# Kernel optimization log

Hardware: AMD Instinct MI355X
Metric: run time of the kernel (lower is better)

## Reference

```python
import jax, jax.numpy as jnp
import numpy as np
import math

B, L, DIM = 2, 2048, 1024
NUM_HEADS, QUANTUM_HEADS, CHUNK = 16, 2, 64
HD = DIM // NUM_HEADS  # 64 == CHUNK (required by the original broadcast)
TH = NUM_HEADS - QUANTUM_HEADS
STEPS = 2048
LN_EPS = 1e-5


def setup_inputs() -> dict:
    key = jax.random.key(0)
    ks = jax.random.split(key, 12)
    inp = {
        'x': jax.random.normal(ks[0], (B, L, DIM), dtype=jnp.float32),
        # to_quantum_state: Linear(HD, 2HD) + LayerNorm(2HD) + Tanh
        'wq1': jax.random.normal(ks[1], (HD, 2 * HD), dtype=jnp.float32) * 0.05,
        'bq1': jnp.zeros((2 * HD,), dtype=jnp.float32),
        'ln_g': jnp.ones((2 * HD,), dtype=jnp.float32),
        'ln_b': jnp.zeros((2 * HD,), dtype=jnp.float32),
        'phase_shifts': jax.random.normal(ks[2], (QUANTUM_HEADS,), dtype=jnp.float32) * 0.02,
        'freqs': jax.random.normal(ks[3], (QUANTUM_HEADS,), dtype=jnp.float32) * 0.02,
        # traditional heads: q/k/v projections, no bias
        'wq': jax.random.normal(ks[4], (DIM, TH * HD), dtype=jnp.float32) * 0.02,
        'wk': jax.random.normal(ks[5], (DIM, TH * HD), dtype=jnp.float32) * 0.02,
        'wv': jax.random.normal(ks[6], (DIM, TH * HD), dtype=jnp.float32) * 0.02,
        # output projection
        'wo': jax.random.normal(ks[7], (DIM, DIM), dtype=jnp.float32) * 0.02,
        'bo': jnp.zeros((DIM,), dtype=jnp.float32),
    }
    return inp


def _quantum_state(t, wq1, bq1, ln_g, ln_b):
    # Linear -> LayerNorm -> Tanh; split into (amp, phase)
    h = t @ wq1 + bq1
    mu = h.mean(-1, keepdims=True)
    var = ((h - mu) ** 2).mean(-1, keepdims=True)
    h = (h - mu) * jax.lax.rsqrt(var + LN_EPS) * ln_g + ln_b
    h = jnp.tanh(h)
    return h[..., :HD], h[..., HD:]


def reference(x, wq1, bq1, ln_g, ln_b, phase_shifts, freqs, wq, wk, wv, wo, bo):
    two_pi = 2.0 * math.pi
    angles = jnp.linspace(0.0, two_pi, STEPS)  # torch.linspace is endpoint-inclusive
    cos_table = jnp.cos(angles)
    inv_sqrt_hd = 1.0 / math.sqrt(HD)
    nc = L // CHUNK

    quantum_outs = []
    for h in range(QUANTUM_HEADS):
        xh = x[..., h * HD:(h + 1) * HD]                       # [B,L,HD]
        amp, phase = _quantum_state(xh, wq1, bq1, ln_g, ln_b)  # each [B,L,HD]
        qa = amp.reshape(B, nc, CHUNK, HD)
        qp = phase.reshape(B, nc, CHUNK, HD)
        # keys/values are truncated to the FIRST `chunk` tokens (original quirk)
        ka = amp[:, :CHUNK]        # [B,CHUNK,HD]
        kp = phase[:, :CHUNK]
        v = xh[:, :CHUNK]
        # phase_diff[b,c,i,j] = qp[b,c,i,j] - kp[b,j,i]  (needs CHUNK == HD)
        pd = (qp - jnp.swapaxes(kp, -1, -2)[:, None]) * freqs[h] + phase_shifts[h]
        idx = jnp.mod(pd / two_pi * STEPS, STEPS).astype(jnp.int32)  # in [0, STEPS)
        interference = cos_table[idx]                          # [B,nc,CHUNK,CHUNK]
        scores = jnp.einsum('bcih,bjh->bcij', qa, ka) * interference
        attn = jax.nn.softmax(scores * inv_sqrt_hd, axis=-1)
        out = jnp.einsum('bcij,bjh->bcih', attn, v).reshape(B, L, HD)
        quantum_outs.append(out)

    # traditional multi-head attention on full x
    q = (x @ wq).reshape(B, L, TH, HD)
    k = (x @ wk).reshape(B, L, TH, HD)
    vv = (x @ wv).reshape(B, L, TH, HD)
    scores = jnp.einsum('bqhd,bkhd->bhqk', q, k) * inv_sqrt_hd
    attn = jax.nn.softmax(scores, axis=-1)
    trad = jnp.einsum('bhqk,bkhd->bqhd', attn, vv).reshape(B, L, TH * HD)

    out = jnp.concatenate(quantum_outs + [trad], axis=-1)  # [B,L,DIM]
    return out @ wo + bo
```

## Files before the change

### kernel.cpp

```cpp
#include <hip/hip_runtime.h>
#include <hip/hip_bf16.h>
#include <math.h>

#define B_ 2
#define L_ 2048
#define DIM_ 1024
#define HD_ 64
#define TH_ 14
#define TWO_PI_F 6.28318530717958647692f
#define QSCALE_F 0.1803368801111204f

typedef __bf16 bf16_t;
typedef __bf16 bf16x8 __attribute__((ext_vector_type(8)));
typedef __bf16 bf16x4 __attribute__((ext_vector_type(4)));
typedef float f32x4 __attribute__((ext_vector_type(4)));
typedef float f32x16 __attribute__((ext_vector_type(16)));
typedef unsigned int u32x2 __attribute__((ext_vector_type(2)));

static __device__ __forceinline__ bf16_t f2b(float f) { return (bf16_t)f; }

static __device__ __forceinline__ float fexp2(float x) {
#if __has_builtin(__builtin_amdgcn_exp2f)
  return __builtin_amdgcn_exp2f(x);
#else
  return exp2f(x);
#endif
}

static __device__ __forceinline__ unsigned int cvtpk(float a, float b) {
  unsigned int r;
  asm("v_cvt_pk_bf16_f32 %0, %1, %2" : "=v"(r) : "v"(a), "v"(b));
  return r;
}

static __device__ __forceinline__ void gl16(const bf16_t* g, bf16_t* l) {
  __builtin_amdgcn_global_load_lds(
      (const __attribute__((address_space(1))) void*)g,
      (__attribute__((address_space(3))) void*)l, 16, 0, 0);
}

static __device__ __forceinline__ void swap32(unsigned int& a, unsigned int& b) {
#if __has_builtin(__builtin_amdgcn_permlane32_swap)
  u32x2 r = __builtin_amdgcn_permlane32_swap(a, b, false, false);
  a = r[0];
  b = r[1];
#else
  const int l = (int)(threadIdx.x & 63);
  unsigned int bp_a = (unsigned int)__builtin_amdgcn_ds_bpermute((l ^ 32) << 2, (int)a);
  unsigned int bp_b = (unsigned int)__builtin_amdgcn_ds_bpermute((l ^ 32) << 2, (int)b);
  unsigned int na = (l < 32) ? a : bp_b;
  unsigned int nb = (l < 32) ? bp_a : b;
  a = na;
  b = nb;
#endif
}

__global__ __launch_bounds__(256)
void k_prep(const float* __restrict__ x, const float* __restrict__ wq1,
            const float* __restrict__ bq1, const float* __restrict__ ln_g,
            const float* __restrict__ ln_b, const float* __restrict__ wq,
            const float* __restrict__ wk, const float* __restrict__ wv,
            const float* __restrict__ wo, bf16_t* __restrict__ xb,
            bf16_t* __restrict__ wt_qkv, bf16_t* __restrict__ wt_o,
            bf16_t* __restrict__ amp_b, float* __restrict__ phase) {
  __shared__ float tile[32][33];
  const int t = threadIdx.x;
  const int bid = blockIdx.x;
  if (bid < 4096) {
    const int i = bid * 256 + t;
    const float4 v4 = ((const float4*)x)[i];
    bf16x4 o = {f2b(v4.x), f2b(v4.y), f2b(v4.z), f2b(v4.w)};
    *(bf16x4*)(xb + 4 * (size_t)i) = o;
  } else if (bid < 7808) {
    const float* W;
    bf16_t* Wt;
    int N, kt, nt;
    if (bid < 6784) {
      int r = bid - 4096;
      const int which = r / 896;
      r -= which * 896;
      W = (which == 0) ? wq : (which == 1) ? wk : wv;
      Wt = wt_qkv + (size_t)which * 896 * 1024;
      N = 896;
      kt = r & 31;
      nt = r >> 5;
    } else {
      const int r = bid - 6784;
      W = wo;
      Wt = wt_o;
      N = 1024;
      kt = r & 31;
      nt = r >> 5;
    }
    const int tx = t & 31, ty = t >> 5;
    const int k0 = kt * 32, n0 = nt * 32;
    #pragma unroll
    for (int i = 0; i < 4; ++i)
      tile[ty + 8 * i][tx] = W[(size_t)(k0 + ty + 8 * i) * N + n0 + tx];
    __syncthreads();
    #pragma unroll
    for (int i = 0; i < 4; ++i)
      Wt[(size_t)(n0 + ty + 8 * i) * 1024 + k0 + tx] = f2b(tile[tx][ty + 8 * i]);
  } else {
    const int gw = ((bid - 7808) * 256 + t) >> 6;
    const int lane = t & 63;
    const int h = gw >> 12;
    const int bl = gw & 4095;
    const float xv = x[(size_t)bl * DIM_ + h * HD_ + lane];
    float acc0 = bq1[lane];
    float acc1 = bq1[64 + lane];
    #pragma unroll 16
    for (int kk = 0; kk < 64; ++kk) {
      const float xk = __shfl(xv, kk, 64);
      acc0 = fmaf(xk, wq1[kk * 128 + lane], acc0);
      acc1 = fmaf(xk, wq1[kk * 128 + 64 + lane], acc1);
    }
    float s = acc0 + acc1;
    #pragma unroll
    for (int off = 32; off > 0; off >>= 1) s += __shfl_xor(s, off, 64);
    const float mu = s * (1.0f / 128.0f);
    const float d0 = acc0 - mu, d1 = acc1 - mu;
    float vsum = d0 * d0 + d1 * d1;
    #pragma unroll
    for (int off = 32; off > 0; off >>= 1) vsum += __shfl_xor(vsum, off, 64);
    const float rstd = rsqrtf(vsum * (1.0f / 128.0f) + 1e-5f);
    const float av = tanhf(d0 * rstd * ln_g[lane] + ln_b[lane]);
    const float pv = tanhf(d1 * rstd * ln_g[64 + lane] + ln_b[64 + lane]);
    const size_t o = ((size_t)h * (B_ * L_) + bl) * HD_ + lane;
    amp_b[o] = f2b(av);
    phase[o] = pv;
  }
}

__global__ __launch_bounds__(256)
void k_mm1q(const bf16_t* __restrict__ A, const bf16_t* __restrict__ Wt,
            bf16_t* __restrict__ qb, bf16_t* __restrict__ kb, bf16_t* __restrict__ vb) {
  __shared__ char smem[32768];
  const int t = threadIdx.x;
  const int lane = t & 63, w = t >> 6;
  const int bid = blockIdx.x;
  const int xcd = bid & 7, slot = bid >> 3;
  bf16_t* Asm = (bf16_t*)smem;
  bf16_t* Bsm = (bf16_t*)(smem + 16384);
  const int wm = w >> 1, wn = w & 1;
  const int l31 = lane & 31, hi = lane >> 5;
  const int m_blk = xcd * 4 + slot / 21;
  const int n_blk = slot % 21;
  const int m0 = m_blk * 128;
  const int n0 = n_blk * 128;
  f32x16 acc[2][2] = {};
  for (int k0 = 0; k0 < 1024; k0 += 64) {
    __syncthreads();
    #pragma unroll
    for (int qc = 0; qc < 4; ++qc) {
      const int idx = t + 256 * qc;
      const int r = idx >> 3, cb = idx & 7;
      const int c = (cb ^ (r & 7)) * 8;
      gl16(A + (size_t)(m0 + r) * 1024 + k0 + c, Asm + w * 512 + qc * 2048);
      gl16(Wt + (size_t)(n0 + r) * 1024 + k0 + c, Bsm + w * 512 + qc * 2048);
    }
    __syncthreads();
    #pragma unroll
    for (int s = 0; s < 4; ++s) {
      const int ra0 = wm * 64 + l31, ra1 = ra0 + 32;
      const int rb0 = wn * 64 + l31, rb1 = rb0 + 32;
      const bf16x8 af0 = *(const bf16x8*)((char*)Asm + ra0 * 128 + (((2 * s + hi) ^ (ra0 & 7)) << 4));
      const bf16x8 af1 = *(const bf16x8*)((char*)Asm + ra1 * 128 + (((2 * s + hi) ^ (ra1 & 7)) << 4));
      const bf16x8 bf0 = *(const bf16x8*)((char*)Bsm + rb0 * 128 + (((2 * s + hi) ^ (rb0 & 7)) << 4));
      const bf16x8 bf1 = *(const bf16x8*)((char*)Bsm + rb1 * 128 + (((2 * s + hi) ^ (rb1 & 7)) << 4));
      acc[0][0] = __builtin_amdgcn_mfma_f32_32x32x16_bf16(bf0, af0, acc[0][0], 0, 0, 0);
      acc[0][1] = __builtin_amdgcn_mfma_f32_32x32x16_bf16(bf1, af0, acc[0][1], 0, 0, 0);
      acc[1][0] = __builtin_amdgcn_mfma_f32_32x32x16_bf16(bf0, af1, acc[1][0], 0, 0, 0);
      acc[1][1] = __builtin_amdgcn_mfma_f32_32x32x16_bf16(bf1, af1, acc[1][1], 0, 0, 0);
    }
  }
  const int n0w = n0 + wn * 64;
  const int which = (n0 >= 1792) ? 2 : (n0 >= 896) ? 1 : 0;
  #pragma unroll
  for (int mi = 0; mi < 2; ++mi) {
    const int m = m0 + wm * 64 + mi * 32 + l31;
    const int bsel = m >> 11, ll = m & 2047;
    #pragma unroll
    for (int ni = 0; ni < 2; ++ni) {
      if (which == 2) {
        #pragma unroll
        for (int rp = 0; rp < 4; ++rp) {
          #pragma unroll
          for (int e = 0; e < 4; ++e) {
            const int nn = n0w + ni * 32 + 8 * rp + 4 * hi + e - 1792;
            const int head = nn >> 6, hd = nn & 63;
            vb[(((size_t)bsel * TH_ + head) * HD_ + hd) * L_ + ll] = f2b(acc[mi][ni][4 * rp + e]);
          }
        }
      } else {
        const float sc = (which == 0) ? QSCALE_F : 1.0f;
        bf16_t* dst = (which == 0) ? qb : kb;
        #pragma unroll
        for (int rp = 0; rp < 4; ++rp) {
          const int nb = n0w + ni * 32 + 8 * rp + 4 * hi;
          const int nn = nb - which * 896;
          const int head = nn >> 6, hd = nn & 63;
          bf16x4 pk;
          #pragma unroll
          for (int e = 0; e < 4; ++e) pk[e] = f2b(acc[mi][ni][4 * rp + e] * sc);
          *(bf16x4*)(dst + (((size_t)bsel * TH_ + head) * L_ + ll) * HD_ + hd) = pk;
        }
      }
    }
  }
}

__global__ __launch_bounds__(256)
void k_mm0(const bf16_t* __restrict__ A, const bf16_t* __restrict__ Wt,
           const float* __restrict__ bias, float* __restrict__ outf) {
  __shared__ bf16_t Asm[128 * 64];
  __shared__ bf16_t Bsm[128 * 64];
  const int t = threadIdx.x;
  const int lane = t & 63, w = t >> 6;
  const int wm = w >> 1, wn = w & 1;
  const int l31 = lane & 31, hi = lane >> 5;
  const int bid = blockIdx.x;
  const int v = (bid & 7) * 32 + (bid >> 3);
  const int m0 = (v & 31) * 128;
  const int n0 = (v >> 5) * 128;
  f32x16 acc[2][2] = {};
  for (int k0 = 0; k0 < 1024; k0 += 64) {
    __syncthreads();
    #pragma unroll
    for (int qc = 0; qc < 4; ++qc) {
      const int idx = t + 256 * qc;
      const int r = idx >> 3, cb = idx & 7;
      const int c = (cb ^ (r & 7)) * 8;
      gl16(A + (size_t)(m0 + r) * 1024 + k0 + c, Asm + w * 512 + qc * 2048);
      gl16(Wt + (size_t)(n0 + r) * 1024 + k0 + c, Bsm + w * 512 + qc * 2048);
    }
    __syncthreads();
    #pragma unroll
    for (int s = 0; s < 4; ++s) {
      const int ra0 = wm * 64 + l31, ra1 = ra0 + 32;
      const int rb0 = wn * 64 + l31, rb1 = rb0 + 32;
      const bf16x8 af0 = *(const bf16x8*)((char*)Asm + ra0 * 128 + (((2 * s + hi) ^ (ra0 & 7)) << 4));
      const bf16x8 af1 = *(const bf16x8*)((char*)Asm + ra1 * 128 + (((2 * s + hi) ^ (ra1 & 7)) << 4));
      const bf16x8 bf0 = *(const bf16x8*)((char*)Bsm + rb0 * 128 + (((2 * s + hi) ^ (rb0 & 7)) << 4));
      const bf16x8 bf1 = *(const bf16x8*)((char*)Bsm + rb1 * 128 + (((2 * s + hi) ^ (rb1 & 7)) << 4));
      acc[0][0] = __builtin_amdgcn_mfma_f32_32x32x16_bf16(bf0, af0, acc[0][0], 0, 0, 0);
      acc[0][1] = __builtin_amdgcn_mfma_f32_32x32x16_bf16(bf1, af0, acc[0][1], 0, 0, 0);
      acc[1][0] = __builtin_amdgcn_mfma_f32_32x32x16_bf16(bf0, af1, acc[1][0], 0, 0, 0);
      acc[1][1] = __builtin_amdgcn_mfma_f32_32x32x16_bf16(bf1, af1, acc[1][1], 0, 0, 0);
    }
  }
  #pragma unroll
  for (int mi = 0; mi < 2; ++mi) {
    const int m = m0 + wm * 64 + mi * 32 + l31;
    #pragma unroll
    for (int ni = 0; ni < 2; ++ni) {
      #pragma unroll
      for (int rp = 0; rp < 4; ++rp) {
        const int nb = n0 + wn * 64 + ni * 32 + 8 * rp + 4 * hi;
        const float4 bv = *(const float4*)&bias[nb];
        float4 r4;
        r4.x = acc[mi][ni][4 * rp + 0] + bv.x;
        r4.y = acc[mi][ni][4 * rp + 1] + bv.y;
        r4.z = acc[mi][ni][4 * rp + 2] + bv.z;
        r4.w = acc[mi][ni][4 * rp + 3] + bv.w;
        *(float4*)&outf[(size_t)m * 1024 + nb] = r4;
      }
    }
  }
}

__global__ __launch_bounds__(512)
void k_flash2(const bf16_t* __restrict__ qg, const bf16_t* __restrict__ kg,
              const bf16_t* __restrict__ vt, bf16_t* __restrict__ catb,
              const bf16_t* __restrict__ A, const bf16_t* __restrict__ amp_b,
              const float* __restrict__ phase, const float* __restrict__ shifts,
              const float* __restrict__ freqs) {
  __shared__ char smem[65536];
  const int t = threadIdx.x;
  const int lane = t & 63, w = t >> 6;
  const int l31 = lane & 31, hi = lane >> 5;
  const int xcd = blockIdx.x & 7, s = blockIdx.x >> 3;
  if (s < 56) {
    const int g2 = w >> 2, wl = w & 3;
    const int tb = xcd * 56 + s;
    const int qblk = tb & 15, bh = tb >> 4;
    const int head = bh % TH_, b = bh / TH_;
    const size_t base = (size_t)bh * (L_ * HD_);
    const int q = qblk * 128 + wl * 32 + l31;
    const int tl = t & 255;
    const int r0 = tl >> 3, cb0 = tl & 7;
    const int r1 = r0 + 32;
    const int c0 = (cb0 ^ (r0 & 7)) * 8;
    const int c1 = (cb0 ^ (r1 & 7)) * 8;
    const int ubase = wl * 512;
    bf16_t* Kg = (bf16_t*)(smem + g2 * 32768);
    bf16_t* Vg = (bf16_t*)(smem + g2 * 32768 + 16384);
    const int kt0 = g2 * 16;

    bf16x8 qf[4];
    #pragma unroll
    for (int slot = 0; slot < 4; ++slot)
      qf[slot] = *(const bf16x8*)(qg + base + (size_t)q * 64 + 16 * slot + 8 * hi);

    f32x16 oT[2] = {};
    float l_acc = 0.0f;

    {
      const bf16_t* ksrc = kg + base + (size_t)kt0 * 64 * 64;
      const bf16_t* vsrc = vt + base + kt0 * 64;
      gl16(ksrc + r0 * 64 + c0, Kg + ubase);
      gl16(ksrc + r1 * 64 + c1, Kg + ubase + 2048);
      gl16(vsrc + (size_t)r0 * L_ + c0, Vg + ubase);
      gl16(vsrc + (size_t)r1 * L_ + c1, Vg + ubase + 2048);
    }
    for (int kt = 0; kt < 16; ++kt) {
      const int cur = kt & 1;
      if (kt < 15) {
        const bf16_t* ksrc = kg + base + (size_t)(kt0 + kt + 1) * 64 * 64;
        const bf16_t* vsrc = vt + base + (kt0 + kt + 1) * 64;
        bf16_t* kd = Kg + (cur ^ 1) * 4096;
        bf16_t* vd = Vg + (cur ^ 1) * 4096;
        gl16(ksrc + r0 * 64 + c0, kd + ubase);
        gl16(ksrc + r1 * 64 + c1, kd + ubase + 2048);
        gl16(vsrc + (size_t)r0 * L_ + c0, vd + ubase);
        gl16(vsrc + (size_t)r1 * L_ + c1, vd + ubase + 2048);
        asm volatile("s_waitcnt vmcnt(4)" ::: "memory");
      } else {
        asm volatile("s_waitcnt vmcnt(0)" ::: "memory");
      }
      __builtin_amdgcn_sched_barrier(0);
      __builtin_amdgcn_s_barrier();
      const char* Kc = (const char*)(Kg + cur * 4096);
      const char* Vc = (const char*)(Vg + cur * 4096);
      f32x16 sT0 = {}, sT1 = {};
      __builtin_amdgcn_s_setprio(1);
      #pragma unroll
      for (int slot = 0; slot < 4; ++slot) {
        const int row0 = l31;
        const int row1 = 32 + l31;
        const bf16x8 kf0 = *(const bf16x8*)(Kc + row0 * 128 + (((2 * slot + hi) ^ (row0 & 7)) << 4));
        const bf16x8 kf1 = *(const bf16x8*)(Kc + row1 * 128 + (((2 * slot + hi) ^ (row1 & 7)) << 4));
        sT0 = __builtin_amdgcn_mfma_f32_32x32x16_bf16(kf0, qf[slot], sT0, 0, 0, 0);
        sT1 = __builtin_amdgcn_mfma_f32_32x32x16_bf16(kf1, qf[slot], sT1, 0, 0, 0);
      }
      __builtin_amdgcn_s_setprio(0);
      unsigned int W0[8], W1[8];
      float la = 0.0f;
      #pragma unroll
      for (int rp = 0; rp < 8; ++rp) {
        const float p00 = fexp2(sT0[2 * rp]);
        const float p01 = fexp2(sT0[2 * rp + 1]);
        const float p10 = fexp2(sT1[2 * rp]);
        const float p11 = fexp2(sT1[2 * rp + 1]);
        la += (p00 + p01) + (p10 + p11);
        W0[rp] = cvtpk(p00, p01);
        W1[rp] = cvtpk(p10, p11);
      }
      l_acc += la;
      unsigned int pb[4][4];
      #pragma unroll
      for (int m1 = 0; m1 < 2; ++m1) {
        unsigned int u, vv;
        u = W0[m1];     vv = W0[2 + m1]; swap32(u, vv); pb[0][m1] = u; pb[0][m1 + 2] = vv;
        u = W0[4 + m1]; vv = W0[6 + m1]; swap32(u, vv); pb[1][m1] = u; pb[1][m1 + 2] = vv;
        u = W1[m1];     vv = W1[2 + m1]; swap32(u, vv); pb[2][m1] = u; pb[2][m1 + 2] = vv;
        u = W1[4 + m1]; vv = W1[6 + m1]; swap32(u, vv); pb[3][m1] = u; pb[3][m1 + 2] = vv;
      }
      __builtin_amdgcn_s_setprio(1);
      #pragma unroll
      for (int slot = 0; slot < 4; ++slot) {
        union { unsigned int u[4]; bf16x8 v8; } pf;
        pf.u[0] = pb[slot][0]; pf.u[1] = pb[slot][1];
        pf.u[2] = pb[slot][2]; pf.u[3] = pb[slot][3];
        #pragma unroll
        for (int dt = 0; dt < 2; ++dt) {
          const int row = 32 * dt + l31;
          const bf16x8 vf = *(const bf16x8*)(Vc + row * 128 + (((2 * slot + hi) ^ (row & 7)) << 4));
          oT[dt] = __builtin_amdgcn_mfma_f32_32x32x16_bf16(vf, pf.v8, oT[dt], 0, 0, 0);
        }
      }
      __builtin_amdgcn_s_setprio(0);
      __builtin_amdgcn_s_barrier();
    }
    const float l_w = l_acc + __shfl_xor(l_acc, 32, 64);
    __syncthreads();
    float* obuf = (float*)(smem + 32768);
    float* lbuf = (float*)smem;
    if (g2 == 1) {
      #pragma unroll
      for (int dt = 0; dt < 2; ++dt)
        #pragma unroll
        for (int e = 0; e < 16; ++e)
          obuf[(dt * 16 + e) * 256 + wl * 64 + lane] = oT[dt][e];
      lbuf[wl * 64 + lane] = l_w;
    }
    __syncthreads();
    if (g2 == 0) {
      const float l_tot = l_w + lbuf[wl * 64 + lane];
      const float inv = 1.0f / l_tot;
      const size_t obase = ((size_t)b * L_ + q) * DIM_ + 128 + head * 64;
      #pragma unroll
      for (int dt = 0; dt < 2; ++dt) {
        #pragma unroll
        for (int rq = 0; rq < 4; ++rq) {
          bf16x4 pk;
          #pragma unroll
          for (int e = 0; e < 4; ++e)
            pk[e] = f2b((oT[dt][4 * rq + e] +
                         obuf[(dt * 16 + 4 * rq + e) * 256 + wl * 64 + lane]) * inv);
          *(bf16x4*)(catb + obase + 32 * dt + 8 * rq + 4 * hi) = pk;
        }
      }
    }
  } else {
    const int g3 = w >> 2, wl = w & 3;
    const int tl = t & 255;
    bf16_t* Kam = (bf16_t*)(smem + g3 * 24576);
    bf16_t* Vt2 = (bf16_t*)(smem + g3 * 24576 + 8192);
    bf16_t* Ps  = (bf16_t*)(smem + g3 * 24576 + 16384);
    const int l15 = lane & 15, g = lane >> 4;
    const int qp = xcd * 8 + (s - 56);
    const int qv = qp * 2 + g3;
    const int c = qv & 31;
    const int hb = qv >> 5;
    const int b = hb & 1;
    const int h = hb >> 1;
    const size_t abase = ((size_t)h * B_ + b) * L_ * HD_;

    {
      const int r0 = tl >> 3, cb0 = tl & 7;
      const int r1 = r0 + 32;
      gl16(amp_b + abase + r0 * 64 + (cb0 ^ (r0 & 7)) * 8, Kam + wl * 512);
      gl16(amp_b + abase + r1 * 64 + (cb0 ^ (r1 & 7)) * 8, Kam + wl * 512 + 2048);
    }
    {
      const int vj = tl >> 2;
      const int vd0 = (tl & 3) * 16;
      const bf16x8 va = *(const bf16x8*)(A + ((size_t)b * L_ + vj) * DIM_ + h * 64 + vd0);
      const bf16x8 vb2 = *(const bf16x8*)(A + ((size_t)b * L_ + vj) * DIM_ + h * 64 + vd0 + 8);
      #pragma unroll
      for (int e = 0; e < 8; ++e) {
        int d = vd0 + e;
        *(bf16_t*)((char*)Vt2 + d * 128 + (((vj >> 3) ^ (d & 7)) << 4) + (vj & 7) * 2) = va[e];
        d = vd0 + 8 + e;
        *(bf16_t*)((char*)Vt2 + d * 128 + (((vj >> 3) ^ (d & 7)) << 4) + (vj & 7) * 2) = vb2[e];
      }
    }
    __syncthreads();

    bf16x8 qf[2];
    {
      const size_t ro = abase + (size_t)(c * 64 + 16 * wl + l15) * 64 + g * 8;
      qf[0] = *(const bf16x8*)(amp_b + ro);
      qf[1] = *(const bf16x8*)(amp_b + ro + 32);
    }
    f32x4 sq[4] = {};
    #pragma unroll
    for (int ks = 0; ks < 2; ++ks) {
      #pragma unroll
      for (int nt = 0; nt < 4; ++nt) {
        const int jr = nt * 16 + l15;
        const bf16x8 kf = *(const bf16x8*)((char*)Kam + jr * 128 + (((ks * 4 + g) ^ (jr & 7)) << 4));
        sq[nt] = __builtin_amdgcn_mfma_f32_16x16x32_bf16(qf[ks], kf, sq[nt], 0, 0, 0);
      }
    }
    const float freq = freqs[h], shift = shifts[h];
    char* PsW = (char*)Ps + wl * 2048;
    float l_acc[4];
    #pragma unroll
    for (int r = 0; r < 4; ++r) {
      const int i_loc = 16 * wl + 4 * g + r;
      const float* qrow = phase + abase + (size_t)(c * 64 + i_loc) * 64;
      const float* krow = phase + abase + i_loc;
      const int row = g * 4 + r;
      float ls = 0.0f;
      #pragma unroll
      for (int nt = 0; nt < 4; ++nt) {
        const int j = nt * 16 + l15;
        const float qp2 = qrow[j];
        const float kp = krow[j * 64];
        const float pd = (qp2 - kp) * freq + shift;
        const float t1 = pd * (2048.0f / TWO_PI_F);
        float mm = fmodf(t1, 2048.0f);
        if (mm < 0.0f) mm += 2048.0f;
        int idx = (int)mm;
        idx = idx > 2047 ? 2047 : idx;
        const float interf = cosf((float)idx * (TWO_PI_F / 2047.0f));
        const float sc = sq[nt][r] * interf * 0.125f;
        const float e = expf(sc);
        ls += e;
        *(bf16_t*)(PsW + row * 128 + (((j >> 3) ^ (row & 7)) << 4) + (j & 7) * 2) = f2b(e);
      }
      #pragma unroll
      for (int off = 1; off < 16; off <<= 1) ls += __shfl_xor(ls, off, 64);
      l_acc[r] = ls;
    }
    f32x4 o[4] = {};
    #pragma unroll
    for (int ks = 0; ks < 2; ++ks) {
      const bf16x8 pa = *(const bf16x8*)(PsW + l15 * 128 + (((ks * 4 + g) ^ (l15 & 7)) << 4));
      #pragma unroll
      for (int nt = 0; nt < 4; ++nt) {
        const int dr = nt * 16 + l15;
        const bf16x8 vf = *(const bf16x8*)((char*)Vt2 + dr * 128 + (((ks * 4 + g) ^ (dr & 7)) << 4));
        o[nt] = __builtin_amdgcn_mfma_f32_16x16x32_bf16(pa, vf, o[nt], 0, 0, 0);
      }
    }
    #pragma unroll
    for (int r = 0; r < 4; ++r) {
      const float inv = 1.0f / l_acc[r];
      const int qrow = c * 64 + 16 * wl + g * 4 + r;
      #pragma unroll
      for (int nt = 0; nt < 4; ++nt)
        catb[((size_t)b * L_ + qrow) * DIM_ + h * 64 + nt * 16 + l15] = f2b(o[nt][r] * inv);
    }
  }
}

extern "C" void kernel_launch(void* const* d_in, const int* in_sizes, int n_in,
                              void* d_out, int out_size, void* d_ws, size_t ws_size,
                              hipStream_t stream) {
  (void)in_sizes; (void)n_in; (void)out_size; (void)ws_size;
  const float* x      = (const float*)d_in[0];
  const float* wq1    = (const float*)d_in[1];
  const float* bq1    = (const float*)d_in[2];
  const float* ln_g   = (const float*)d_in[3];
  const float* ln_b   = (const float*)d_in[4];
  const float* shifts = (const float*)d_in[5];
  const float* freqs  = (const float*)d_in[6];
  const float* wq     = (const float*)d_in[7];
  const float* wk     = (const float*)d_in[8];
  const float* wv     = (const float*)d_in[9];
  const float* wo     = (const float*)d_in[10];
  const float* bo     = (const float*)d_in[11];
  float* out = (float*)d_out;

  char* p = (char*)d_ws;
  bf16_t* amp_b  = (bf16_t*)p; p += (size_t)2 * B_ * L_ * HD_ * 2;
  float* phase   = (float*)p;  p += (size_t)2 * B_ * L_ * HD_ * 4;
  bf16_t* xb     = (bf16_t*)p; p += (size_t)B_ * L_ * DIM_ * 2;
  bf16_t* wt_qkv = (bf16_t*)p; p += (size_t)2688 * 1024 * 2;
  bf16_t* wt_o   = (bf16_t*)p; p += (size_t)1024 * 1024 * 2;
  bf16_t* qb     = (bf16_t*)p; p += (size_t)B_ * TH_ * L_ * HD_ * 2;
  bf16_t* kb     = (bf16_t*)p; p += (size_t)B_ * TH_ * L_ * HD_ * 2;
  bf16_t* vtb    = (bf16_t*)p; p += (size_t)B_ * TH_ * L_ * HD_ * 2;
  bf16_t* catb   = (bf16_t*)p;

  k_prep<<<dim3(9856), dim3(256), 0, stream>>>(x, wq1, bq1, ln_g, ln_b,
                                               wq, wk, wv, wo,
                                               xb, wt_qkv, wt_o, amp_b, phase);
  k_mm1q<<<dim3(672), dim3(256), 0, stream>>>(xb, wt_qkv, qb, kb, vtb);
  k_flash2<<<dim3(512), dim3(512), 0, stream>>>(qb, kb, vtb, catb,
                                                xb, amp_b, phase, shifts, freqs);
  k_mm0<<<dim3(256), dim3(256), 0, stream>>>(catb, wt_o, bo, out);
}
```

Measured before the change: 119.9 us.

## Triple-buffer K/V tiles in flash kernel and remap mm0 tiles per XCD

The flash attention loop goes from double to triple buffering of its K/V shared-memory tiles. Loads are now issued two tiles ahead, right after the barrier, and the trailing barrier at the end of each iteration is removed. The aim is to hide global-load latency and cut synchronisation. Shared memory grows from 64KB to 96KB per block, which may stop two 512-thread blocks from sharing a CU. Separately, the output-projection GEMM now assigns tiles so each XCD gets a contiguous band of M rows, which should improve L2 reuse of A.

```diff
diff --git a/kernel.cpp b/kernel.cpp
--- a/kernel.cpp
+++ b/kernel.cpp
@@ -220,9 +220,9 @@
   const int wm = w >> 1, wn = w & 1;
   const int l31 = lane & 31, hi = lane >> 5;
   const int bid = blockIdx.x;
-  const int v = (bid & 7) * 32 + (bid >> 3);
-  const int m0 = (v & 31) * 128;
-  const int n0 = (v >> 5) * 128;
+  const int xcd = bid & 7, slot = bid >> 3;
+  const int m0 = (xcd * 4 + (slot >> 3)) * 128;
+  const int n0 = (slot & 7) * 128;
   f32x16 acc[2][2] = {};
   for (int k0 = 0; k0 < 1024; k0 += 64) {
     __syncthreads();
@@ -275,7 +275,7 @@
               const bf16_t* __restrict__ A, const bf16_t* __restrict__ amp_b,
               const float* __restrict__ phase, const float* __restrict__ shifts,
               const float* __restrict__ freqs) {
-  __shared__ char smem[65536];
+  __shared__ char smem[98304];
   const int t = threadIdx.x;
   const int lane = t & 63, w = t >> 6;
   const int l31 = lane & 31, hi = lane >> 5;
@@ -293,9 +293,20 @@
     const int c0 = (cb0 ^ (r0 & 7)) * 8;
     const int c1 = (cb0 ^ (r1 & 7)) * 8;
     const int ubase = wl * 512;
-    bf16_t* Kg = (bf16_t*)(smem + g2 * 32768);
-    bf16_t* Vg = (bf16_t*)(smem + g2 * 32768 + 16384);
+    bf16_t* Kb = (bf16_t*)(smem + g2 * 49152);
+    bf16_t* Vb = (bf16_t*)(smem + g2 * 49152 + 24576);
     const int kt0 = g2 * 16;
+
+    auto STAGE = [&](int slot, int tile) {
+      const bf16_t* ksrc = kg + base + (size_t)tile * 4096;
+      const bf16_t* vsrc = vt + base + tile * 64;
+      bf16_t* kd = Kb + slot * 4096;
+      bf16_t* vd = Vb + slot * 4096;
+      gl16(ksrc + r0 * 64 + c0, kd + ubase);
+      gl16(ksrc + r1 * 64 + c1, kd + ubase + 2048);
+      gl16(vsrc + (size_t)r0 * L_ + c0, vd + ubase);
+      gl16(vsrc + (size_t)r1 * L_ + c1, vd + ubase + 2048);
+    };
 
     bf16x8 qf[4];
     #pragma unroll
@@ -305,33 +316,23 @@
     f32x16 oT[2] = {};
     float l_acc = 0.0f;
 
-    {
-      const bf16_t* ksrc = kg + base + (size_t)kt0 * 64 * 64;
-      const bf16_t* vsrc = vt + base + kt0 * 64;
-      gl16(ksrc + r0 * 64 + c0, Kg + ubase);
-      gl16(ksrc + r1 * 64 + c1, Kg + ubase + 2048);
-      gl16(vsrc + (size_t)r0 * L_ + c0, Vg + ubase);
-      gl16(vsrc + (size_t)r1 * L_ + c1, Vg + ubase + 2048);
-    }
+    STAGE(0, kt0 + 0);
+    STAGE(1, kt0 + 1);
+    int cur = 0;
     for (int kt = 0; kt < 16; ++kt) {
-      const int cur = kt & 1;
       if (kt < 15) {
-        const bf16_t* ksrc = kg + base + (size_t)(kt0 + kt + 1) * 64 * 64;
-        const bf16_t* vsrc = vt + base + (kt0 + kt + 1) * 64;
-        bf16_t* kd = Kg + (cur ^ 1) * 4096;
-        bf16_t* vd = Vg + (cur ^ 1) * 4096;
-        gl16(ksrc + r0 * 64 + c0, kd + ubase);
-        gl16(ksrc + r1 * 64 + c1, kd + ubase + 2048);
-        gl16(vsrc + (size_t)r0 * L_ + c0, vd + ubase);
-        gl16(vsrc + (size_t)r1 * L_ + c1, vd + ubase + 2048);
         asm volatile("s_waitcnt vmcnt(4)" ::: "memory");
       } else {
         asm volatile("s_waitcnt vmcnt(0)" ::: "memory");
       }
       __builtin_amdgcn_sched_barrier(0);
       __builtin_amdgcn_s_barrier();
-      const char* Kc = (const char*)(Kg + cur * 4096);
-      const char* Vc = (const char*)(Vg + cur * 4096);
+      if (kt < 14) {
+        const int nslot = (cur == 0) ? 2 : cur - 1;
+        STAGE(nslot, kt0 + kt + 2);
+      }
+      const char* Kc = (const char*)(Kb + cur * 4096);
+      const char* Vc = (const char*)(Vb + cur * 4096);
       f32x16 sT0 = {}, sT1 = {};
       __builtin_amdgcn_s_setprio(1);
       #pragma unroll
@@ -380,11 +381,11 @@
         }
       }
       __builtin_amdgcn_s_setprio(0);
-      __builtin_amdgcn_s_barrier();
+      cur = (cur == 2) ? 0 : cur + 1;
     }
     const float l_w = l_acc + __shfl_xor(l_acc, 32, 64);
     __syncthreads();
-    float* obuf = (float*)(smem + 32768);
+    float* obuf = (float*)(smem + 49152);
     float* lbuf = (float*)smem;
     if (g2 == 1) {
       #pragma unroll
```

Measured after the change: 124.6 us. 3.9% more time.

## Double-buffer LDS tiles in projection GEMMs to overlap global loads with MFMA

Applied to the files above, without the earlier changes.

Both the QKV projection GEMM and the output projection GEMM now keep two LDS buffers and issue the next K-tile's global-to-LDS loads before computing on the current tile. This uses one barrier per iteration instead of two, so load latency can be hidden behind MFMA work. The output GEMM also changes its block-to-tile mapping so each XCD covers a contiguous band of M rows. LDS per block doubles to 64KB, which may reduce the number of blocks resident per CU.

```diff
diff --git a/kernel.cpp b/kernel.cpp
--- a/kernel.cpp
+++ b/kernel.cpp
@@ -135,39 +135,50 @@
 __global__ __launch_bounds__(256)
 void k_mm1q(const bf16_t* __restrict__ A, const bf16_t* __restrict__ Wt,
             bf16_t* __restrict__ qb, bf16_t* __restrict__ kb, bf16_t* __restrict__ vb) {
-  __shared__ char smem[32768];
+  __shared__ char smem[65536];
   const int t = threadIdx.x;
   const int lane = t & 63, w = t >> 6;
   const int bid = blockIdx.x;
   const int xcd = bid & 7, slot = bid >> 3;
   bf16_t* Asm = (bf16_t*)smem;
-  bf16_t* Bsm = (bf16_t*)(smem + 16384);
+  bf16_t* Bsm = (bf16_t*)(smem + 32768);
   const int wm = w >> 1, wn = w & 1;
   const int l31 = lane & 31, hi = lane >> 5;
   const int m_blk = xcd * 4 + slot / 21;
   const int n_blk = slot % 21;
   const int m0 = m_blk * 128;
   const int n0 = n_blk * 128;
+  const int sr = t >> 3, scb = t & 7;
+  const int sc = (scb ^ (sr & 7)) * 8;
+
+  auto STAGE = [&](int buf, int k0) {
+    #pragma unroll
+    for (int qc = 0; qc < 4; ++qc) {
+      const int r = sr + 32 * qc;
+      const int c = (scb ^ (r & 7)) * 8;
+      gl16(A + (size_t)(m0 + r) * 1024 + k0 + c, Asm + buf * 8192 + w * 512 + qc * 2048);
+      gl16(Wt + (size_t)(n0 + r) * 1024 + k0 + c, Bsm + buf * 8192 + w * 512 + qc * 2048);
+    }
+  };
+  (void)sc;
+
   f32x16 acc[2][2] = {};
-  for (int k0 = 0; k0 < 1024; k0 += 64) {
-    __syncthreads();
-    #pragma unroll
-    for (int qc = 0; qc < 4; ++qc) {
-      const int idx = t + 256 * qc;
-      const int r = idx >> 3, cb = idx & 7;
-      const int c = (cb ^ (r & 7)) * 8;
-      gl16(A + (size_t)(m0 + r) * 1024 + k0 + c, Asm + w * 512 + qc * 2048);
-      gl16(Wt + (size_t)(n0 + r) * 1024 + k0 + c, Bsm + w * 512 + qc * 2048);
-    }
-    __syncthreads();
+  STAGE(0, 0);
+  for (int kt = 0; kt < 16; ++kt) {
+    asm volatile("s_waitcnt vmcnt(0)" ::: "memory");
+    __builtin_amdgcn_sched_barrier(0);
+    __builtin_amdgcn_s_barrier();
+    if (kt < 15) STAGE((kt & 1) ^ 1, (kt + 1) * 64);
+    const char* Ac = (const char*)(Asm + (kt & 1) * 8192);
+    const char* Bc = (const char*)(Bsm + (kt & 1) * 8192);
     #pragma unroll
     for (int s = 0; s < 4; ++s) {
       const int ra0 = wm * 64 + l31, ra1 = ra0 + 32;
       const int rb0 = wn * 64 + l31, rb1 = rb0 + 32;
-      const bf16x8 af0 = *(const bf16x8*)((char*)Asm + ra0 * 128 + (((2 * s + hi) ^ (ra0 & 7)) << 4));
-      const bf16x8 af1 = *(const bf16x8*)((char*)Asm + ra1 * 128 + (((2 * s + hi) ^ (ra1 & 7)) << 4));
-      const bf16x8 bf0 = *(const bf16x8*)((char*)Bsm + rb0 * 128 + (((2 * s + hi) ^ (rb0 & 7)) << 4));
-      const bf16x8 bf1 = *(const bf16x8*)((char*)Bsm + rb1 * 128 + (((2 * s + hi) ^ (rb1 & 7)) << 4));
+      const bf16x8 af0 = *(const bf16x8*)(Ac + ra0 * 128 + (((2 * s + hi) ^ (ra0 & 7)) << 4));
+      const bf16x8 af1 = *(const bf16x8*)(Ac + ra1 * 128 + (((2 * s + hi) ^ (ra1 & 7)) << 4));
+      const bf16x8 bf0 = *(const bf16x8*)(Bc + rb0 * 128 + (((2 * s + hi) ^ (rb0 & 7)) << 4));
+      const bf16x8 bf1 = *(const bf16x8*)(Bc + rb1 * 128 + (((2 * s + hi) ^ (rb1 & 7)) << 4));
       acc[0][0] = __builtin_amdgcn_mfma_f32_32x32x16_bf16(bf0, af0, acc[0][0], 0, 0, 0);
       acc[0][1] = __builtin_amdgcn_mfma_f32_32x32x16_bf16(bf1, af0, acc[0][1], 0, 0, 0);
       acc[1][0] = __builtin_amdgcn_mfma_f32_32x32x16_bf16(bf0, af1, acc[1][0], 0, 0, 0);
@@ -193,7 +204,7 @@
           }
         }
       } else {
-        const float sc = (which == 0) ? QSCALE_F : 1.0f;
+        const float sc2 = (which == 0) ? QSCALE_F : 1.0f;
         bf16_t* dst = (which == 0) ? qb : kb;
         #pragma unroll
         for (int rp = 0; rp < 4; ++rp) {
@@ -202,7 +213,7 @@
           const int head = nn >> 6, hd = nn & 63;
           bf16x4 pk;
           #pragma unroll
-          for (int e = 0; e < 4; ++e) pk[e] = f2b(acc[mi][ni][4 * rp + e] * sc);
+          for (int e = 0; e < 4; ++e) pk[e] = f2b(acc[mi][ni][4 * rp + e] * sc2);
           *(bf16x4*)(dst + (((size_t)bsel * TH_ + head) * L_ + ll) * HD_ + hd) = pk;
         }
       }
@@ -213,36 +224,46 @@
 __global__ __launch_bounds__(256)
 void k_mm0(const bf16_t* __restrict__ A, const bf16_t* __restrict__ Wt,
            const float* __restrict__ bias, float* __restrict__ outf) {
-  __shared__ bf16_t Asm[128 * 64];
-  __shared__ bf16_t Bsm[128 * 64];
+  __shared__ char smem[65536];
+  bf16_t* Asm = (bf16_t*)smem;
+  bf16_t* Bsm = (bf16_t*)(smem + 32768);
   const int t = threadIdx.x;
   const int lane = t & 63, w = t >> 6;
   const int wm = w >> 1, wn = w & 1;
   const int l31 = lane & 31, hi = lane >> 5;
   const int bid = blockIdx.x;
-  const int v = (bid & 7) * 32 + (bid >> 3);
-  const int m0 = (v & 31) * 128;
-  const int n0 = (v >> 5) * 128;
+  const int xcd = bid & 7, slot = bid >> 3;
+  const int m0 = (xcd * 4 + (slot >> 3)) * 128;
+  const int n0 = (slot & 7) * 128;
+  const int sr = t >> 3, scb = t & 7;
+
+  auto STAGE = [&](int buf, int k0) {
+    #pragma unroll
+    for (int qc = 0; qc < 4; ++qc) {
+      const int r = sr + 32 * qc;
+      const int c = (scb ^ (r & 7)) * 8;
+      gl16(A + (size_t)(m0 + r) * 1024 + k0 + c, Asm + buf * 8192 + w * 512 + qc * 2048);
+      gl16(Wt + (size_t)(n0 + r) * 1024 + k0 + c, Bsm + buf * 8192 + w * 512 + qc * 2048);
+    }
+  };
+
   f32x16 acc[2][2] = {};
-  for (int k0 = 0; k0 < 1024; k0 += 64) {
-    __syncthreads();
-    #pragma unroll
-    for (int qc = 0; qc < 4; ++qc) {
-      const int idx = t + 256 * qc;
-      const int r = idx >> 3, cb = idx & 7;
-      const int c = (cb ^ (r & 7)) * 8;
-      gl16(A + (size_t)(m0 + r) * 1024 + k0 + c, Asm + w * 512 + qc * 2048);
-      gl16(Wt + (size_t)(n0 + r) * 1024 + k0 + c, Bsm + w * 512 + qc * 2048);
-    }
-    __syncthreads();
+  STAGE(0, 0);
+  for (int kt = 0; kt < 16; ++kt) {
+    asm volatile("s_waitcnt vmcnt(0)" ::: "memory");
+    __builtin_amdgcn_sched_barrier(0);
+    __builtin_amdgcn_s_barrier();
+    if (kt < 15) STAGE((kt & 1) ^ 1, (kt + 1) * 64);
+    const char* Ac = (const char*)(Asm + (kt & 1) * 8192);
+    const char* Bc = (const char*)(Bsm + (kt & 1) * 8192);
     #pragma unroll
     for (int s = 0; s < 4; ++s) {
       const int ra0 = wm * 64 + l31, ra1 = ra0 + 32;
       const int rb0 = wn * 64 + l31, rb1 = rb0 + 32;
-      const bf16x8 af0 = *(const bf16x8*)((char*)Asm + ra0 * 128 + (((2 * s + hi) ^ (ra0 & 7)) << 4));
-      const bf16x8 af1 = *(const bf16x8*)((char*)Asm + ra1 * 128 + (((2 * s + hi) ^ (ra1 & 7)) << 4));
-      const bf16x8 bf0 = *(const bf16x8*)((char*)Bsm + rb0 * 128 + (((2 * s + hi) ^ (rb0 & 7)) << 4));
-      const bf16x8 bf1 = *(const bf16x8*)((char*)Bsm + rb1 * 128 + (((2 * s + hi) ^ (rb1 & 7)) << 4));
+      const bf16x8 af0 = *(const bf16x8*)(Ac + ra0 * 128 + (((2 * s + hi) ^ (ra0 & 7)) << 4));
+      const bf16x8 af1 = *(const bf16x8*)(Ac + ra1 * 128 + (((2 * s + hi) ^ (ra1 & 7)) << 4));
+      const bf16x8 bf0 = *(const bf16x8*)(Bc + rb0 * 128 + (((2 * s + hi) ^ (rb0 & 7)) << 4));
+      const bf16x8 bf1 = *(const bf16x8*)(Bc + rb1 * 128 + (((2 * s + hi) ^ (rb1 & 7)) << 4));
       acc[0][0] = __builtin_amdgcn_mfma_f32_32x32x16_bf16(bf0, af0, acc[0][0], 0, 0, 0);
       acc[0][1] = __builtin_amdgcn_mfma_f32_32x32x16_bf16(bf1, af0, acc[0][1], 0, 0, 0);
       acc[1][0] = __builtin_amdgcn_mfma_f32_32x32x16_bf16(bf0, af1, acc[1][0], 0, 0, 0);
```

Measured after the change: 116.5 us. 1.03x faster.
